# Optimization experiments

Hardware: AMD Instinct MI355X
Metric: run time of the kernel (lower is better)

## Reference

```python
import jax, jax.numpy as jnp
import numpy as np

B, T, H, IN, D = 256, 64, 256, 2, 8

def _gru_cell(x, h, Wih, Whh, bih, bhh):
    gi = x @ Wih.T + bih          # [B,3H]
    gh = h @ Whh.T + bhh
    ir, iz, inn = jnp.split(gi, 3, axis=-1)
    hr, hz, hn = jnp.split(gh, 3, axis=-1)
    r = jax.nn.sigmoid(ir + hr)
    z = jax.nn.sigmoid(iz + hz)
    n = jnp.tanh(inn + r * hn)
    return (1.0 - z) * n + z * h

def _gru2(x, h, p):
    # h: [2,B,H]; p: 8-tuple of layer-0 then layer-1 GRU params
    h0 = _gru_cell(x, h[0], p[0], p[1], p[2], p[3])
    h1 = _gru_cell(h0, h[1], p[4], p[5], p[6], p[7])
    return jnp.stack([h0, h1], axis=0)

def _attend(h_new, buf, i, attn_W, v_W, fc_W, fc_b):
    # h_new: [2,B,H] fresh RNN hidden; buf: [B,T,2,H] history of hiddens
    s = h_new.transpose(1, 0, 2)                            # [B,2,H]
    es = jnp.einsum('blh,gh->blg', s, attn_W[:, :H])        # s half of cat(s,hiddens)
    eh = jnp.einsum('bjlh,gh->bjlg', buf, attn_W[:, H:])    # hiddens half
    energy = jnp.tanh(es[:, None] + eh)                     # [B,T,2,H]
    logits = jnp.einsum('bjlg,og->bjlo', energy, v_W)       # [B,T,2,2]
    mask = (jnp.arange(buf.shape[1]) <= i)[None, :, None, None]
    logits = jnp.where(mask, logits, jnp.float32(-1e30))
    m = logits.max(axis=(1, 2), keepdims=True)              # softmax over all 2*(i+1) history slots
    e = jnp.exp(logits - m)
    a = e / e.sum(axis=(1, 2), keepdims=True)
    c = jnp.einsum('bjlo,bjlh->obh', a, buf)                # [2,B,H] == bmm(a,hiddens).transpose(0,1)
    h_cat = jnp.concatenate([c, h_new], axis=-1)            # [2,B,2H]
    return h_cat @ fc_W.T + fc_b                            # [2,B,H]

def setup_inputs():
    key = jax.random.key(0)
    ks = jax.random.split(key, 32)
    def u(k, shape, fan):
        b = 1.0 / np.sqrt(fan)
        return jax.random.uniform(k, shape, jnp.float32, -b, b)
    inp = {'received': jax.random.normal(ks[0], (B, T, IN), jnp.float32)}
    i = 1
    for g in ('g1', 'g2'):
        inp[g + '_Wih0'] = u(ks[i], (3 * H, IN), H); i += 1
        inp[g + '_Whh0'] = u(ks[i], (3 * H, H), H); i += 1
        inp[g + '_bih0'] = u(ks[i], (3 * H,), H); i += 1
        inp[g + '_bhh0'] = u(ks[i], (3 * H,), H); i += 1
        inp[g + '_Wih1'] = u(ks[i], (3 * H, H), H); i += 1
        inp[g + '_Whh1'] = u(ks[i], (3 * H, H), H); i += 1
        inp[g + '_bih1'] = u(ks[i], (3 * H,), H); i += 1
        inp[g + '_bhh1'] = u(ks[i], (3 * H,), H); i += 1
    inp['fc_W'] = u(ks[i], (H, 2 * H), 2 * H); i += 1
    inp['fc_b'] = u(ks[i], (H,), 2 * H); i += 1
    inp['attn_W'] = u(ks[i], (H, 2 * H), 2 * H); i += 1
    inp['v_W'] = u(ks[i], (2, H), H); i += 1
    inp['out_W'] = u(ks[i], (1, 2 * H), 2 * H); i += 1
    inp['out_b'] = u(ks[i], (1,), 2 * H); i += 1
    return inp

def reference(received, g1_Wih0, g1_Whh0, g1_bih0, g1_bhh0, g1_Wih1, g1_Whh1, g1_bih1, g1_bhh1,
              g2_Wih0, g2_Whh0, g2_bih0, g2_bhh0, g2_Wih1, g2_Whh1, g2_bih1, g2_bhh1,
              fc_W, fc_b, attn_W, v_W, out_W, out_b):
    p1 = (g1_Wih0, g1_Whh0, g1_bih0, g1_bhh0, g1_Wih1, g1_Whh1, g1_bih1, g1_bhh1)
    p2 = (g2_Wih0, g2_Whh0, g2_bih0, g2_bhh0, g2_Wih1, g2_Whh1, g2_bih1, g2_bhh1)
    b, t = received.shape[0], received.shape[1]
    h_init = jnp.zeros((2, b, H), received.dtype)
    buf_init = jnp.zeros((b, t, 2, H), received.dtype)

    def step(carry, inp):
        h1, h2, b1, b2 = carry
        x, i = inp
        h1n = _gru2(x, h1, p1)
        h2n = _gru2(x, h2, p2)
        b1 = b1.at[:, i].set(h1n.transpose(1, 0, 2))
        b2 = b2.at[:, i].set(h2n.transpose(1, 0, 2))
        h1a = _attend(h1n, b1, i, attn_W, v_W, fc_W, fc_b)
        h2a = _attend(h2n, b2, i, attn_W, v_W, fc_W, fc_b)
        return (h1a, h2a, b1, b2), (h1n[1], h2n[1])

    xs = (received.transpose(1, 0, 2), jnp.arange(t))
    _, (o1, o2) = jax.lax.scan(step, (h_init, h_init, buf_init, buf_init), xs)
    out1 = o1.transpose(1, 0, 2)   # [B,T,H] = concat of per-step top-layer GRU outputs
    out2 = o2.transpose(1, 0, 2)
    ar = jnp.arange(t)
    idx = jnp.where(ar >= t - D - 1, t - 1, ar + D)   # delayed stream-2 features
    rnn_out = jnp.concatenate([out1, out2[:, idx]], axis=-1)  # [B,T,2H]
    return jax.nn.sigmoid(rnn_out @ out_W.T + out_b)          # [B,T,1]
```

## Files before the change

kernel.cpp:

```cpp
#include <hip/hip_runtime.h>

#define BATCH 256
#define TT    64
#define HH    256
#define DD    8

#define BW    4
#define NTHR  512
#define NBLK  (2 * (BATCH / BW))

typedef __attribute__((ext_vector_type(8))) short bfrag;
typedef __attribute__((ext_vector_type(4))) float f4;
typedef __attribute__((ext_vector_type(4))) unsigned int uv4;
typedef __attribute__((ext_vector_type(2))) unsigned int uv2;

#define SWZ(g) ((((g) & 31) << 3) | ((g) >> 5))

__device__ __forceinline__ float rcpf(float x) { return __builtin_amdgcn_rcpf(x); }
__device__ __forceinline__ float sigf(float x) { return rcpf(1.0f + __expf(-x)); }
__device__ __forceinline__ float tanh_fast(float x) {
  const float e = __expf(-2.0f * x);
  return __builtin_fmaf(2.0f, rcpf(1.0f + e), -1.0f);
}
__device__ __forceinline__ unsigned short f2bf(float f) {
  union { float f; unsigned int u; } v; v.f = f;
  return (unsigned short)((v.u + 0x7fffu + ((v.u >> 16) & 1u)) >> 16);
}
__device__ __forceinline__ float bf_lo(unsigned int u) {
  union { unsigned int u; float f; } v; v.u = u << 16; return v.f;
}
__device__ __forceinline__ float bf_hi(unsigned int u) {
  union { unsigned int u; float f; } v; v.u = u & 0xffff0000u; return v.f;
}
__device__ __forceinline__ bfrag zero_frag() {
  bfrag r;
#pragma unroll
  for (int x = 0; x < 8; x++) r[x] = 0;
  return r;
}
__device__ __forceinline__ f4 mfma16(bfrag a, bfrag b, f4 c) {
  return __builtin_amdgcn_mfma_f32_16x16x32_bf16(a, b, c, 0, 0, 0);
}

#define W1_ELEMS  196608
#define STACK_W   (3 * W1_ELEMS)
#define B3_OFF    (2 * STACK_W)
#define B4_OFF    (B3_OFF + 131072)
#define WF_TOTAL  (B4_OFF + 131072)

__global__ __launch_bounds__(256) void prep_weights(
    const float* __restrict__ g1_Whh0, const float* __restrict__ g1_Wih1, const float* __restrict__ g1_Whh1,
    const float* __restrict__ g2_Whh0, const float* __restrict__ g2_Wih1, const float* __restrict__ g2_Whh1,
    const float* __restrict__ attn_W, const float* __restrict__ fc_W,
    unsigned short* __restrict__ wf) {
  const int id = blockIdx.x * 256 + threadIdx.x;
  if (id >= WF_TOTAL) return;
  float src;
  if (id < 2 * STACK_W) {
    const int s = id / STACK_W, r = id % STACK_W;
    const int mm = r / W1_ELEMS, e = r % W1_ELEMS;
    const int j = e & 7, lane = (e >> 3) & 63, c = (e >> 9) & 7, t = e >> 12;
    const int nt = t / 3, g = t % 3;
    const int n = nt * 16 + (lane & 15);
    const int k = c * 32 + ((lane >> 4) << 3) + j;
    const float* W = (mm == 0) ? (s ? g2_Whh0 : g1_Whh0)
                   : (mm == 1) ? (s ? g2_Wih1 : g1_Wih1)
                               : (s ? g2_Whh1 : g1_Whh1);
    src = W[(g * 256 + n) * 256 + k];
  } else if (id < B4_OFF) {
    const int e = id - B3_OFF;
    const int j = e & 7, lane = (e >> 3) & 63, c = (e >> 9) & 7, t = e >> 12;
    const int n = t * 16 + (lane & 15);
    const int k = c * 32 + ((lane >> 4) << 3) + j;
    src = (n < 256) ? attn_W[n * 512 + k] : attn_W[(n - 256) * 512 + 256 + k];
  } else {
    const int e = id - B4_OFF;
    const int j = e & 7, lane = (e >> 3) & 63, c = (e >> 9) & 15, t = e >> 13;
    const int n = t * 16 + (lane & 15);
    const int k = c * 32 + ((lane >> 4) << 3) + j;
    src = fc_W[n * 512 + k];
  }
  wf[id] = f2bf(src);
}

__global__ __launch_bounds__(NTHR, 2) void gru_attn(
    const float* __restrict__ received,
    const float* __restrict__ g1_Wih0, const float* __restrict__ g1_bih0, const float* __restrict__ g1_bhh0,
    const float* __restrict__ g1_bih1, const float* __restrict__ g1_bhh1,
    const float* __restrict__ g2_Wih0, const float* __restrict__ g2_bih0, const float* __restrict__ g2_bhh0,
    const float* __restrict__ g2_bih1, const float* __restrict__ g2_bhh1,
    const float* __restrict__ fc_b, const float* __restrict__ v_W, const float* __restrict__ out_W,
    const unsigned short* __restrict__ wf,
    unsigned short* __restrict__ buf_g, unsigned short* __restrict__ ehb_g,
    float* __restrict__ ws_p) {
  const int tid  = threadIdx.x;
  const int lane = tid & 63, wave = tid >> 6;
  const int col  = lane & 15, q = lane >> 4;
  const int s    = blockIdx.x & 1;
  const int b0   = (blockIdx.x >> 1) * BW;

  const float* Wih0 = s ? g2_Wih0 : g1_Wih0;
  const float* bih0 = s ? g2_bih0 : g1_bih0;
  const float* bhh0 = s ? g2_bhh0 : g1_bhh0;
  const float* bih1 = s ? g2_bih1 : g1_bih1;
  const float* bhh1 = s ? g2_bhh1 : g1_bhh1;

  const bfrag* W1  = (const bfrag*)(wf + (size_t)s * STACK_W);
  const bfrag* W2I = W1 + W1_ELEMS / 8;
  const bfrag* W2H = W2I + W1_ELEMS / 8;
  const bfrag* B3  = (const bfrag*)(wf + B3_OFF);
  const bfrag* B4  = (const bfrag*)(wf + B4_OFF);

  unsigned short* buf = buf_g + (size_t)s * BATCH * TT * 2 * HH;
  unsigned short* ehb = ehb_g + (size_t)s * BATCH * TT * 2 * HH;
  float* pp = ws_p + (size_t)s * BATCH * TT;

  float wxr0v[2], wxr1v[2], wxz0v[2], wxz1v[2], wxn0v[2], wxn1v[2];
  float br0v[2], bz0v[2], bni0v[2], bnh0v[2];
  float br1v[2], bz1v[2], bni1v[2], bnh1v[2];
  float fcbv[2], owvv[2];
#pragma unroll
  for (int r2 = 0; r2 < 2; r2++) {
    const int nm = (wave + 8 * r2) * 16 + col;
    wxr0v[r2] = Wih0[nm * 2];         wxr1v[r2] = Wih0[nm * 2 + 1];
    wxz0v[r2] = Wih0[(256 + nm) * 2]; wxz1v[r2] = Wih0[(256 + nm) * 2 + 1];
    wxn0v[r2] = Wih0[(512 + nm) * 2]; wxn1v[r2] = Wih0[(512 + nm) * 2 + 1];
    br0v[r2]  = bih0[nm] + bhh0[nm];
    bz0v[r2]  = bih0[256 + nm] + bhh0[256 + nm];
    bni0v[r2] = bih0[512 + nm]; bnh0v[r2] = bhh0[512 + nm];
    br1v[r2]  = bih1[nm] + bhh1[nm];
    bz1v[r2]  = bih1[256 + nm] + bhh1[256 + nm];
    bni1v[r2] = bih1[512 + nm]; bnh1v[r2] = bhh1[512 + nm];
    fcbv[r2]  = fc_b[nm];
    owvv[r2]  = out_W[s * HH + nm];
  }

  __shared__ float          hf[8 * 260] __attribute__((aligned(16)));
  __shared__ unsigned short hb[8 * 264] __attribute__((aligned(16)));
  __shared__ unsigned short hnb[8 * 264] __attribute__((aligned(16)));
  __shared__ float          es_s[8 * 264] __attribute__((aligned(16)));
  __shared__ unsigned short cacb[8 * 264] __attribute__((aligned(16)));
  __shared__ float          lp[TT * 4 * 2 * 2];
  __shared__ float          vw_s[512];
  __shared__ float          cpart[2 * 2 * 4 * 256] __attribute__((aligned(16)));
  __shared__ float          pw_s[32];
  __shared__ float          sinv_s[8];

  for (int x = tid; x < 8 * 260; x += NTHR) hf[x] = 0.0f;
  for (int x = tid; x < 8 * 264; x += NTHR) hb[x] = 0;
  { const int o = tid >> 8, g = tid & 255; vw_s[o * 256 + SWZ(g)] = v_W[tid]; }
  __syncthreads();

#pragma unroll 1
  for (int i = 0; i < TT; ++i) {
    float2 xv[BW];
#pragma unroll
    for (int b = 0; b < BW; b++) xv[b] = ((const float2*)received)[(size_t)(b0 + b) * TT + i];

    {
      bfrag a0[8];
#pragma unroll
      for (int c = 0; c < 8; c++)
        a0[c] = (col < BW) ? *(const bfrag*)&hb[col * 264 + c * 32 + q * 8] : zero_frag();
#pragma unroll
      for (int r2 = 0; r2 < 2; r2++) {
        const int nt16 = wave + 8 * r2;
        bfrag bb[24];
#pragma unroll
        for (int c = 0; c < 8; c++) {
          bb[c]      = W1[((nt16 * 3 + 0) * 8 + c) * 64 + lane];
          bb[8 + c]  = W1[((nt16 * 3 + 1) * 8 + c) * 64 + lane];
          bb[16 + c] = W1[((nt16 * 3 + 2) * 8 + c) * 64 + lane];
        }
        f4 aR = {0, 0, 0, 0}, aZ = {0, 0, 0, 0}, aN = {0, 0, 0, 0};
#pragma unroll
        for (int c = 0; c < 8; c++) {
          aR = mfma16(a0[c], bb[c], aR);
          aZ = mfma16(a0[c], bb[8 + c], aZ);
          aN = mfma16(a0[c], bb[16 + c], aN);
        }
        if (lane < 16) {
          const int nm = nt16 * 16 + col;
#pragma unroll
          for (int reg = 0; reg < 4; reg++) {
            const int b = reg;
            const float rr = sigf(xv[b].x * wxr0v[r2] + xv[b].y * wxr1v[r2] + br0v[r2] + aR[reg]);
            const float zz = sigf(xv[b].x * wxz0v[r2] + xv[b].y * wxz1v[r2] + bz0v[r2] + aZ[reg]);
            const float nn = tanh_fast(xv[b].x * wxn0v[r2] + xv[b].y * wxn1v[r2] + bni0v[r2] +
                                       rr * (aN[reg] + bnh0v[r2]));
            const float hn0 = (1.0f - zz) * nn + zz * hf[b * 260 + nm];
            const unsigned short hv = f2bf(hn0);
            hnb[b * 264 + nm] = hv;
            buf[((size_t)(b0 + b) * (TT * 2) + i * 2 + 0) * HH + nm] = hv;
          }
        }
      }
    }
    __syncthreads();

    {
      bfrag ai[8], ah[8];
#pragma unroll
      for (int c = 0; c < 8; c++) {
        ai[c] = (col < BW) ? *(const bfrag*)&hnb[col * 264 + c * 32 + q * 8] : zero_frag();
        ah[c] = (col < BW) ? *(const bfrag*)&hb[(4 + col) * 264 + c * 32 + q * 8] : zero_frag();
      }
      float pv[4] = {0.f, 0.f, 0.f, 0.f};
#pragma unroll
      for (int r2 = 0; r2 < 2; r2++) {
        const int nt16 = wave + 8 * r2;
        bfrag bb[24];
#pragma unroll
        for (int c = 0; c < 8; c++) {
          bb[c]      = W2I[((nt16 * 3 + 0) * 8 + c) * 64 + lane];
          bb[8 + c]  = W2I[((nt16 * 3 + 1) * 8 + c) * 64 + lane];
          bb[16 + c] = W2I[((nt16 * 3 + 2) * 8 + c) * 64 + lane];
        }
        f4 iR = {0, 0, 0, 0}, iZ = {0, 0, 0, 0}, iN = {0, 0, 0, 0};
#pragma unroll
        for (int c = 0; c < 8; c++) {
          iR = mfma16(ai[c], bb[c], iR);
          iZ = mfma16(ai[c], bb[8 + c], iZ);
          iN = mfma16(ai[c], bb[16 + c], iN);
        }
#pragma unroll
        for (int c = 0; c < 8; c++) {
          bb[c]      = W2H[((nt16 * 3 + 0) * 8 + c) * 64 + lane];
          bb[8 + c]  = W2H[((nt16 * 3 + 1) * 8 + c) * 64 + lane];
          bb[16 + c] = W2H[((nt16 * 3 + 2) * 8 + c) * 64 + lane];
        }
        f4 hR = {0, 0, 0, 0}, hZ = {0, 0, 0, 0}, hN = {0, 0, 0, 0};
#pragma unroll
        for (int c = 0; c < 8; c++) {
          hR = mfma16(ah[c], bb[c], hR);
          hZ = mfma16(ah[c], bb[8 + c], hZ);
          hN = mfma16(ah[c], bb[16 + c], hN);
        }
        if (lane < 16) {
          const int nm = nt16 * 16 + col;
#pragma unroll
          for (int reg = 0; reg < 4; reg++) {
            const int b = reg;
            const float rr = sigf(iR[reg] + hR[reg] + br1v[r2]);
            const float zz = sigf(iZ[reg] + hZ[reg] + bz1v[r2]);
            const float nn = tanh_fast(iN[reg] + bni1v[r2] + rr * (hN[reg] + bnh1v[r2]));
            const float hn1 = (1.0f - zz) * nn + zz * hf[(4 + b) * 260 + nm];
            const unsigned short hv = f2bf(hn1);
            hnb[(4 + b) * 264 + nm] = hv;
            buf[((size_t)(b0 + b) * (TT * 2) + i * 2 + 1) * HH + nm] = hv;
            pv[reg] += hn1 * owvv[r2];
          }
        }
      }
#pragma unroll
      for (int reg = 0; reg < 4; reg++) {
#pragma unroll
        for (int d = 1; d < 16; d <<= 1) pv[reg] += __shfl_xor(pv[reg], d, 64);
      }
      if (lane == 0) {
#pragma unroll
        for (int reg = 0; reg < 4; reg++) pw_s[wave * 4 + reg] = pv[reg];
      }
    }
    __syncthreads();

    {
      bfrag a3[8];
#pragma unroll
      for (int c = 0; c < 8; c++)
        a3[c] = (col < 8) ? *(const bfrag*)&hnb[col * 264 + c * 32 + q * 8] : zero_frag();
#pragma unroll
      for (int tt = 0; tt < 4; tt++) {
        const int t = wave * 4 + tt;
        bfrag bb[8];
#pragma unroll
        for (int c = 0; c < 8; c++) bb[c] = B3[(t * 8 + c) * 64 + lane];
        f4 acc = {0, 0, 0, 0};
#pragma unroll
        for (int c = 0; c < 8; c++) acc = mfma16(a3[c], bb[c], acc);
        if (lane < 32) {
          const int n = t * 16 + col;
#pragma unroll
          for (int reg = 0; reg < 4; reg++) {
            const int m = q * 4 + reg;
            const int l = m >> 2, b = m & 3;
            if (t < 16) es_s[(b * 2 + l) * 264 + SWZ(n)] = acc[reg];
            else ehb[((size_t)(b0 + b) * (TT * 2) + i * 2 + l) * HH + (n - 256)] = f2bf(acc[reg]);
          }
        }
      }
      if (tid < 4) {
        float ss = 0.0f;
#pragma unroll
        for (int w = 0; w < 8; w++) ss += pw_s[w * 4 + tid];
        pp[(size_t)(b0 + tid) * TT + i] = ss;
      }
    }
    __syncthreads();

    {
      const int nslot = 64 * (i + 1);
      int slot = tid;
      uv4 cur[4];
      if (slot < nslot) {
        const uv4* ep = (const uv4*)(ehb + ((size_t)(b0 + ((slot >> 3) & 3)) * (TT * 2) +
                                            (slot >> 6) * 2 + ((slot >> 5) & 1)) * HH + (slot & 7) * 32);
#pragma unroll
        for (int u = 0; u < 4; u++) cur[u] = __builtin_nontemporal_load(ep + u);
      }
      for (; slot < nslot; slot += NTHR) {
        const int snext = slot + NTHR;
        uv4 nxt[4];
        if (snext < nslot) {
          const uv4* ep2 = (const uv4*)(ehb + ((size_t)(b0 + ((snext >> 3) & 3)) * (TT * 2) +
                                               (snext >> 6) * 2 + ((snext >> 5) & 1)) * HH + (snext & 7) * 32);
#pragma unroll
          for (int u = 0; u < 4; u++) nxt[u] = __builtin_nontemporal_load(ep2 + u);
        } else {
#pragma unroll
          for (int u = 0; u < 4; u++) nxt[u] = cur[u];
        }
        const int g8 = slot & 7;
        const int b  = (slot >> 3) & 3;
        const int l  = (slot >> 5) & 1;
        const int j  = slot >> 6;
        const int eb = (b * 2 + l) * 264;
        float l0 = 0.0f, l1 = 0.0f;
#pragma unroll
        for (int u = 0; u < 4; u++) {
#pragma unroll
          for (int k = 0; k < 4; k++) {
            const int m = u * 8 + k * 2;
            const float e0 = tanh_fast(es_s[eb + (m * 8 + g8)] + bf_lo(cur[u][k]));
            const float e1 = tanh_fast(es_s[eb + ((m + 1) * 8 + g8)] + bf_hi(cur[u][k]));
            l0 = fmaf(e0, vw_s[m * 8 + g8], fmaf(e1, vw_s[(m + 1) * 8 + g8], l0));
            l1 = fmaf(e0, vw_s[256 + m * 8 + g8], fmaf(e1, vw_s[256 + (m + 1) * 8 + g8], l1));
          }
        }
#pragma unroll
        for (int d = 1; d < 8; d <<= 1) { l0 += __shfl_xor(l0, d, 64); l1 += __shfl_xor(l1, d, 64); }
        if (g8 == 0) {
          lp[((j * 4 + b) * 2 + l) * 2 + 0] = __expf(l0);
          lp[((j * 4 + b) * 2 + l) * 2 + 1] = __expf(l1);
        }
#pragma unroll
        for (int u = 0; u < 4; u++) cur[u] = nxt[u];
      }
    }
    __syncthreads();

    {
      {
        const int b = wave >> 1, o = wave & 1;
        const int jl2 = 2 * (i + 1);
        const int jl0 = lane, jl1 = lane + 64;
        float sa = 0.0f;
        if (jl0 < jl2) sa += lp[((jl0 >> 1) * 4 + b) * 4 + (jl0 & 1) * 2 + o];
        if (jl1 < jl2) sa += lp[((jl1 >> 1) * 4 + b) * 4 + (jl1 & 1) * 2 + o];
#pragma unroll
        for (int d = 1; d < 64; d <<= 1) sa += __shfl_xor(sa, d, 64);
        if (lane == 0) sinv_s[b * 2 + o] = rcpf(sa);
      }
      const int h4   = tid & 63;
      const int jpar = (tid >> 6) & 1;
      const int cb   = tid >> 7;
      const uv2* bp = (const uv2*)(buf + ((size_t)(b0 + cb) * (TT * 2)) * HH);
      float c00 = 0.f, c01 = 0.f, c02 = 0.f, c03 = 0.f;
      float c10 = 0.f, c11 = 0.f, c12 = 0.f, c13 = 0.f;
      uv2 aj0 = {0, 0}, aj1 = {0, 0}, bj0 = {0, 0}, bj1 = {0, 0};
      int j = jpar;
      if (j <= i) {
        aj0 = __builtin_nontemporal_load(bp + (j * 2 + 0) * 64 + h4);
        aj1 = __builtin_nontemporal_load(bp + (j * 2 + 1) * 64 + h4);
        bj0 = __builtin_nontemporal_load(bp + ((j + 2) * 2 + 0) * 64 + h4);
        bj1 = __builtin_nontemporal_load(bp + ((j + 2) * 2 + 1) * 64 + h4);
      }
      for (; j <= i; j += 2) {
        uv2 cj0 = {0, 0}, cj1 = {0, 0};
        if (j + 4 <= i) {
          cj0 = __builtin_nontemporal_load(bp + ((j + 4) * 2 + 0) * 64 + h4);
          cj1 = __builtin_nontemporal_load(bp + ((j + 4) * 2 + 1) * 64 + h4);
        }
#pragma unroll
        for (int l = 0; l < 2; l++) {
          const uv2 u = l ? aj1 : aj0;
          const float e0 = lp[((j * 4 + cb) * 2 + l) * 2 + 0];
          const float e1 = lp[((j * 4 + cb) * 2 + l) * 2 + 1];
          const float v0 = bf_lo(u[0]), v1 = bf_hi(u[0]);
          const float v2 = bf_lo(u[1]), v3 = bf_hi(u[1]);
          c00 = fmaf(e0, v0, c00); c01 = fmaf(e0, v1, c01);
          c02 = fmaf(e0, v2, c02); c03 = fmaf(e0, v3, c03);
          c10 = fmaf(e1, v0, c10); c11 = fmaf(e1, v1, c11);
          c12 = fmaf(e1, v2, c12); c13 = fmaf(e1, v3, c13);
        }
        aj0 = bj0; aj1 = bj1; bj0 = cj0; bj1 = cj1;
      }
      ((float4*)&cpart[((jpar * 2 + 0) * 4 + cb) * 256])[h4] = make_float4(c00, c01, c02, c03);
      ((float4*)&cpart[((jpar * 2 + 1) * 4 + cb) * 256])[h4] = make_float4(c10, c11, c12, c13);
    }
    __syncthreads();

    for (int x = tid; x < 2 * BW * HH; x += NTHR) {
      const int g = x & 255, b = (x >> 8) & 3, o = x >> 10;
      const float v = (cpart[(o * 4 + b) * 256 + g] + cpart[((2 + o) * 4 + b) * 256 + g]) *
                      sinv_s[b * 2 + o];
      cacb[(o * 4 + b) * 264 + g] = f2bf(v);
    }
    __syncthreads();

    {
      bfrag a4[16];
      if (col < 8) {
#pragma unroll
        for (int c = 0; c < 8; c++) {
          a4[c]     = *(const bfrag*)&cacb[col * 264 + c * 32 + q * 8];
          a4[c + 8] = *(const bfrag*)&hnb[col * 264 + c * 32 + q * 8];
        }
      } else {
#pragma unroll
        for (int c = 0; c < 16; c++) a4[c] = zero_frag();
      }
#pragma unroll
      for (int r2 = 0; r2 < 2; r2++) {
        const int t16 = wave + 8 * r2;
        bfrag bb[16];
#pragma unroll
        for (int c = 0; c < 16; c++) bb[c] = B4[(t16 * 16 + c) * 64 + lane];
        f4 acc = {0, 0, 0, 0};
#pragma unroll
        for (int c = 0; c < 16; c++) acc = mfma16(a4[c], bb[c], acc);
        if (lane < 32) {
          const int nm = t16 * 16 + col;
#pragma unroll
          for (int reg = 0; reg < 4; reg++) {
            const int m = q * 4 + reg;
            const float v = acc[reg] + fcbv[r2];
            hf[m * 260 + nm] = v;
            hb[m * 264 + nm] = f2bf(v);
          }
        }
      }
    }
    __syncthreads();
  }
}

__global__ __launch_bounds__(256) void final_combine(const float* __restrict__ ws_p,
                                                     const float* __restrict__ out_b,
                                                     float* __restrict__ out) {
  const int gidx = blockIdx.x * blockDim.x + threadIdx.x;
  if (gidx >= BATCH * TT) return;
  const int b = gidx >> 6;
  const int t = gidx & 63;
  const int idx = (t >= TT - DD - 1) ? (TT - 1) : (t + DD);
  const float* p1 = ws_p;
  const float* p2 = ws_p + (size_t)BATCH * TT;
  const float v = p1[(size_t)b * TT + t] + p2[(size_t)b * TT + idx] + out_b[0];
  out[gidx] = 1.0f / (1.0f + __expf(-v));
}

extern "C" void kernel_launch(void* const* d_in, const int* in_sizes, int n_in,
                              void* d_out, int out_size, void* d_ws, size_t ws_size,
                              hipStream_t stream) {
  const float* received = (const float*)d_in[0];
  const float* g1_Wih0 = (const float*)d_in[1];
  const float* g1_Whh0 = (const float*)d_in[2];
  const float* g1_bih0 = (const float*)d_in[3];
  const float* g1_bhh0 = (const float*)d_in[4];
  const float* g1_Wih1 = (const float*)d_in[5];
  const float* g1_Whh1 = (const float*)d_in[6];
  const float* g1_bih1 = (const float*)d_in[7];
  const float* g1_bhh1 = (const float*)d_in[8];
  const float* g2_Wih0 = (const float*)d_in[9];
  const float* g2_Whh0 = (const float*)d_in[10];
  const float* g2_bih0 = (const float*)d_in[11];
  const float* g2_bhh0 = (const float*)d_in[12];
  const float* g2_Wih1 = (const float*)d_in[13];
  const float* g2_Whh1 = (const float*)d_in[14];
  const float* g2_bih1 = (const float*)d_in[15];
  const float* g2_bhh1 = (const float*)d_in[16];
  const float* fc_W   = (const float*)d_in[17];
  const float* fc_b   = (const float*)d_in[18];
  const float* attn_W = (const float*)d_in[19];
  const float* v_W    = (const float*)d_in[20];
  const float* out_W  = (const float*)d_in[21];
  const float* out_b  = (const float*)d_in[22];

  float* ws_p = (float*)d_ws;
  unsigned short* buf = (unsigned short*)(ws_p + 2 * BATCH * TT);
  unsigned short* ehb = buf + (size_t)2 * BATCH * TT * 2 * HH;
  unsigned short* wf  = ehb + (size_t)2 * BATCH * TT * 2 * HH;

  hipLaunchKernelGGL(prep_weights, dim3((WF_TOTAL + 255) / 256), dim3(256), 0, stream,
                     g1_Whh0, g1_Wih1, g1_Whh1, g2_Whh0, g2_Wih1, g2_Whh1,
                     attn_W, fc_W, wf);

  hipLaunchKernelGGL(gru_attn, dim3(NBLK), dim3(NTHR), 0, stream,
                     received,
                     g1_Wih0, g1_bih0, g1_bhh0, g1_bih1, g1_bhh1,
                     g2_Wih0, g2_bih0, g2_bhh0, g2_bih1, g2_bhh1,
                     fc_b, v_W, out_W, wf, buf, ehb, ws_p);

  hipLaunchKernelGGL(final_combine, dim3((BATCH * TT + 255) / 256), dim3(256), 0, stream,
                     ws_p, out_b, (float*)d_out);
}
```

Before: 5.926 ms.

## Halve batch per block and keep hidden history buffer in LDS

Drops the batch rows per block from 4 to 2, which doubles the grid to 256 blocks, and keeps each block's full hidden-state history (64×2×2×256 bf16, 128 KB) in shared memory instead of global memory. The context-vector accumulation now reads that LDS history directly, with one thread per (batch, h) pair, and folds the softmax normalisation sum into the same loop. This removes the cpart/sinv staging and one barrier. The ehb stores become nontemporal. The cost is that half the MFMA rows sit unused in each 16-row tile, the weights are streamed again per block twice as often, and the large LDS footprint probably limits occupancy to one block per CU.

New measurement: 8.111 ms. 36.9% more time.

```diff
diff --git a/kernel.cpp b/kernel.cpp
--- a/kernel.cpp
+++ b/kernel.cpp
@@ -5,14 +5,13 @@
 #define HH    256
 #define DD    8
 
-#define BW    4
+#define BW    2
 #define NTHR  512
 #define NBLK  (2 * (BATCH / BW))
 
 typedef __attribute__((ext_vector_type(8))) short bfrag;
 typedef __attribute__((ext_vector_type(4))) float f4;
 typedef __attribute__((ext_vector_type(4))) unsigned int uv4;
-typedef __attribute__((ext_vector_type(2))) unsigned int uv2;
 
 #define SWZ(g) ((((g) & 31) << 3) | ((g) >> 5))
 
@@ -25,6 +24,9 @@
 __device__ __forceinline__ unsigned short f2bf(float f) {
   union { float f; unsigned int u; } v; v.f = f;
   return (unsigned short)((v.u + 0x7fffu + ((v.u >> 16) & 1u)) >> 16);
+}
+__device__ __forceinline__ float bf2f(unsigned short u) {
+  union { unsigned int u; float f; } v; v.u = ((unsigned int)u) << 16; return v.f;
 }
 __device__ __forceinline__ float bf_lo(unsigned int u) {
   union { unsigned int u; float f; } v; v.u = u << 16; return v.f;
@@ -91,8 +93,7 @@
     const float* __restrict__ g2_bih1, const float* __restrict__ g2_bhh1,
     const float* __restrict__ fc_b, const float* __restrict__ v_W, const float* __restrict__ out_W,
     const unsigned short* __restrict__ wf,
-    unsigned short* __restrict__ buf_g, unsigned short* __restrict__ ehb_g,
-    float* __restrict__ ws_p) {
+    unsigned short* __restrict__ ehb_g, float* __restrict__ ws_p) {
   const int tid  = threadIdx.x;
   const int lane = tid & 63, wave = tid >> 6;
   const int col  = lane & 15, q = lane >> 4;
@@ -111,7 +112,6 @@
   const bfrag* B3  = (const bfrag*)(wf + B3_OFF);
   const bfrag* B4  = (const bfrag*)(wf + B4_OFF);
 
-  unsigned short* buf = buf_g + (size_t)s * BATCH * TT * 2 * HH;
   unsigned short* ehb = ehb_g + (size_t)s * BATCH * TT * 2 * HH;
   float* pp = ws_p + (size_t)s * BATCH * TT;
 
@@ -135,19 +135,18 @@
     owvv[r2]  = out_W[s * HH + nm];
   }
 
-  __shared__ float          hf[8 * 260] __attribute__((aligned(16)));
-  __shared__ unsigned short hb[8 * 264] __attribute__((aligned(16)));
-  __shared__ unsigned short hnb[8 * 264] __attribute__((aligned(16)));
-  __shared__ float          es_s[8 * 264] __attribute__((aligned(16)));
-  __shared__ unsigned short cacb[8 * 264] __attribute__((aligned(16)));
-  __shared__ float          lp[TT * 4 * 2 * 2];
+  __shared__ unsigned short bufL[TT * 2 * 2 * 256];
+  __shared__ float          hf[4 * 260] __attribute__((aligned(16)));
+  __shared__ unsigned short hb[4 * 264] __attribute__((aligned(16)));
+  __shared__ unsigned short hnb[4 * 264] __attribute__((aligned(16)));
+  __shared__ float          es_s[4 * 264] __attribute__((aligned(16)));
+  __shared__ unsigned short cacb[4 * 264] __attribute__((aligned(16)));
+  __shared__ float          lp[TT * 2 * 2 * 2];
   __shared__ float          vw_s[512];
-  __shared__ float          cpart[2 * 2 * 4 * 256] __attribute__((aligned(16)));
-  __shared__ float          pw_s[32];
-  __shared__ float          sinv_s[8];
-
-  for (int x = tid; x < 8 * 260; x += NTHR) hf[x] = 0.0f;
-  for (int x = tid; x < 8 * 264; x += NTHR) hb[x] = 0;
+  __shared__ float          pw_s[16];
+
+  for (int x = tid; x < 4 * 260; x += NTHR) hf[x] = 0.0f;
+  for (int x = tid; x < 4 * 264; x += NTHR) hb[x] = 0;
   { const int o = tid >> 8, g = tid & 255; vw_s[o * 256 + SWZ(g)] = v_W[tid]; }
   __syncthreads();
 
@@ -182,7 +181,7 @@
         if (lane < 16) {
           const int nm = nt16 * 16 + col;
 #pragma unroll
-          for (int reg = 0; reg < 4; reg++) {
+          for (int reg = 0; reg < BW; reg++) {
             const int b = reg;
             const float rr = sigf(xv[b].x * wxr0v[r2] + xv[b].y * wxr1v[r2] + br0v[r2] + aR[reg]);
             const float zz = sigf(xv[b].x * wxz0v[r2] + xv[b].y * wxz1v[r2] + bz0v[r2] + aZ[reg]);
@@ -191,7 +190,7 @@
             const float hn0 = (1.0f - zz) * nn + zz * hf[b * 260 + nm];
             const unsigned short hv = f2bf(hn0);
             hnb[b * 264 + nm] = hv;
-            buf[((size_t)(b0 + b) * (TT * 2) + i * 2 + 0) * HH + nm] = hv;
+            bufL[((i * 2 + 0) * 2 + b) * 256 + nm] = hv;
           }
         }
       }
@@ -203,9 +202,9 @@
 #pragma unroll
       for (int c = 0; c < 8; c++) {
         ai[c] = (col < BW) ? *(const bfrag*)&hnb[col * 264 + c * 32 + q * 8] : zero_frag();
-        ah[c] = (col < BW) ? *(const bfrag*)&hb[(4 + col) * 264 + c * 32 + q * 8] : zero_frag();
-      }
-      float pv[4] = {0.f, 0.f, 0.f, 0.f};
+        ah[c] = (col < BW) ? *(const bfrag*)&hb[(2 + col) * 264 + c * 32 + q * 8] : zero_frag();
+      }
+      float pv[BW] = {0.f, 0.f};
 #pragma unroll
       for (int r2 = 0; r2 < 2; r2++) {
         const int nt16 = wave + 8 * r2;
@@ -239,27 +238,27 @@
         if (lane < 16) {
           const int nm = nt16 * 16 + col;
 #pragma unroll
-          for (int reg = 0; reg < 4; reg++) {
+          for (int reg = 0; reg < BW; reg++) {
             const int b = reg;
             const float rr = sigf(iR[reg] + hR[reg] + br1v[r2]);
             const float zz = sigf(iZ[reg] + hZ[reg] + bz1v[r2]);
             const float nn = tanh_fast(iN[reg] + bni1v[r2] + rr * (hN[reg] + bnh1v[r2]));
-            const float hn1 = (1.0f - zz) * nn + zz * hf[(4 + b) * 260 + nm];
+            const float hn1 = (1.0f - zz) * nn + zz * hf[(2 + b) * 260 + nm];
             const unsigned short hv = f2bf(hn1);
-            hnb[(4 + b) * 264 + nm] = hv;
-            buf[((size_t)(b0 + b) * (TT * 2) + i * 2 + 1) * HH + nm] = hv;
+            hnb[(2 + b) * 264 + nm] = hv;
+            bufL[((i * 2 + 1) * 2 + b) * 256 + nm] = hv;
             pv[reg] += hn1 * owvv[r2];
           }
         }
       }
 #pragma unroll
-      for (int reg = 0; reg < 4; reg++) {
+      for (int reg = 0; reg < BW; reg++) {
 #pragma unroll
         for (int d = 1; d < 16; d <<= 1) pv[reg] += __shfl_xor(pv[reg], d, 64);
       }
       if (lane == 0) {
 #pragma unroll
-        for (int reg = 0; reg < 4; reg++) pw_s[wave * 4 + reg] = pv[reg];
+        for (int reg = 0; reg < BW; reg++) pw_s[wave * 2 + reg] = pv[reg];
       }
     }
     __syncthreads();
@@ -268,7 +267,7 @@
       bfrag a3[8];
 #pragma unroll
       for (int c = 0; c < 8; c++)
-        a3[c] = (col < 8) ? *(const bfrag*)&hnb[col * 264 + c * 32 + q * 8] : zero_frag();
+        a3[c] = (col < 4) ? *(const bfrag*)&hnb[col * 264 + c * 32 + q * 8] : zero_frag();
 #pragma unroll
       for (int tt = 0; tt < 4; tt++) {
         const int t = wave * 4 + tt;
@@ -278,33 +277,34 @@
         f4 acc = {0, 0, 0, 0};
 #pragma unroll
         for (int c = 0; c < 8; c++) acc = mfma16(a3[c], bb[c], acc);
-        if (lane < 32) {
+        if (lane < 16) {
           const int n = t * 16 + col;
 #pragma unroll
           for (int reg = 0; reg < 4; reg++) {
-            const int m = q * 4 + reg;
-            const int l = m >> 2, b = m & 3;
+            const int l = reg >> 1, b = reg & 1;
             if (t < 16) es_s[(b * 2 + l) * 264 + SWZ(n)] = acc[reg];
-            else ehb[((size_t)(b0 + b) * (TT * 2) + i * 2 + l) * HH + (n - 256)] = f2bf(acc[reg]);
+            else __builtin_nontemporal_store(
+                     f2bf(acc[reg]),
+                     &ehb[((size_t)(b0 + b) * (TT * 2) + i * 2 + l) * HH + (n - 256)]);
           }
         }
       }
-      if (tid < 4) {
+      if (tid < BW) {
         float ss = 0.0f;
 #pragma unroll
-        for (int w = 0; w < 8; w++) ss += pw_s[w * 4 + tid];
+        for (int w = 0; w < 8; w++) ss += pw_s[w * 2 + tid];
         pp[(size_t)(b0 + tid) * TT + i] = ss;
       }
     }
     __syncthreads();
 
     {
-      const int nslot = 64 * (i + 1);
+      const int nslot = 32 * (i + 1);
       int slot = tid;
       uv4 cur[4];
       if (slot < nslot) {
-        const uv4* ep = (const uv4*)(ehb + ((size_t)(b0 + ((slot >> 3) & 3)) * (TT * 2) +
-                                            (slot >> 6) * 2 + ((slot >> 5) & 1)) * HH + (slot & 7) * 32);
+        const uv4* ep = (const uv4*)(ehb + ((size_t)(b0 + ((slot >> 3) & 1)) * (TT * 2) +
+                                            (slot >> 5) * 2 + ((slot >> 4) & 1)) * HH + (slot & 7) * 32);
 #pragma unroll
         for (int u = 0; u < 4; u++) cur[u] = __builtin_nontemporal_load(ep + u);
       }
@@ -312,8 +312,8 @@
         const int snext = slot + NTHR;
         uv4 nxt[4];
         if (snext < nslot) {
-          const uv4* ep2 = (const uv4*)(ehb + ((size_t)(b0 + ((snext >> 3) & 3)) * (TT * 2) +
-                                               (snext >> 6) * 2 + ((snext >> 5) & 1)) * HH + (snext & 7) * 32);
+          const uv4* ep2 = (const uv4*)(ehb + ((size_t)(b0 + ((snext >> 3) & 1)) * (TT * 2) +
+                                               (snext >> 5) * 2 + ((snext >> 4) & 1)) * HH + (snext & 7) * 32);
 #pragma unroll
           for (int u = 0; u < 4; u++) nxt[u] = __builtin_nontemporal_load(ep2 + u);
         } else {
@@ -321,9 +321,9 @@
           for (int u = 0; u < 4; u++) nxt[u] = cur[u];
         }
         const int g8 = slot & 7;
-        const int b  = (slot >> 3) & 3;
-        const int l  = (slot >> 5) & 1;
-        const int j  = slot >> 6;
+        const int b  = (slot >> 3) & 1;
+        const int l  = (slot >> 4) & 1;
+        const int j  = slot >> 5;
         const int eb = (b * 2 + l) * 264;
         float l0 = 0.0f, l1 = 0.0f;
 #pragma unroll
@@ -340,8 +340,8 @@
 #pragma unroll
         for (int d = 1; d < 8; d <<= 1) { l0 += __shfl_xor(l0, d, 64); l1 += __shfl_xor(l1, d, 64); }
         if (g8 == 0) {
-          lp[((j * 4 + b) * 2 + l) * 2 + 0] = __expf(l0);
-          lp[((j * 4 + b) * 2 + l) * 2 + 1] = __expf(l1);
+          lp[((j * 2 + b) * 2 + l) * 2 + 0] = __expf(l0);
+          lp[((j * 2 + b) * 2 + l) * 2 + 1] = __expf(l1);
         }
 #pragma unroll
         for (int u = 0; u < 4; u++) cur[u] = nxt[u];
@@ -350,67 +350,27 @@
     __syncthreads();
 
     {
-      {
-        const int b = wave >> 1, o = wave & 1;
-        const int jl2 = 2 * (i + 1);
-        const int jl0 = lane, jl1 = lane + 64;
-        float sa = 0.0f;
-        if (jl0 < jl2) sa += lp[((jl0 >> 1) * 4 + b) * 4 + (jl0 & 1) * 2 + o];
-        if (jl1 < jl2) sa += lp[((jl1 >> 1) * 4 + b) * 4 + (jl1 & 1) * 2 + o];
-#pragma unroll
-        for (int d = 1; d < 64; d <<= 1) sa += __shfl_xor(sa, d, 64);
-        if (lane == 0) sinv_s[b * 2 + o] = rcpf(sa);
-      }
-      const int h4   = tid & 63;
-      const int jpar = (tid >> 6) & 1;
-      const int cb   = tid >> 7;
-      const uv2* bp = (const uv2*)(buf + ((size_t)(b0 + cb) * (TT * 2)) * HH);
-      float c00 = 0.f, c01 = 0.f, c02 = 0.f, c03 = 0.f;
-      float c10 = 0.f, c11 = 0.f, c12 = 0.f, c13 = 0.f;
-      uv2 aj0 = {0, 0}, aj1 = {0, 0}, bj0 = {0, 0}, bj1 = {0, 0};
-      int j = jpar;
-      if (j <= i) {
-        aj0 = __builtin_nontemporal_load(bp + (j * 2 + 0) * 64 + h4);
-        aj1 = __builtin_nontemporal_load(bp + (j * 2 + 1) * 64 + h4);
-        bj0 = __builtin_nontemporal_load(bp + ((j + 2) * 2 + 0) * 64 + h4);
-        bj1 = __builtin_nontemporal_load(bp + ((j + 2) * 2 + 1) * 64 + h4);
-      }
-      for (; j <= i; j += 2) {
-        uv2 cj0 = {0, 0}, cj1 = {0, 0};
-        if (j + 4 <= i) {
-          cj0 = __builtin_nontemporal_load(bp + ((j + 4) * 2 + 0) * 64 + h4);
-          cj1 = __builtin_nontemporal_load(bp + ((j + 4) * 2 + 1) * 64 + h4);
-        }
+      const int cb = tid >> 8;
+      const int h  = tid & 255;
+      float c0 = 0.f, c1 = 0.f, ss0 = 0.f, ss1 = 0.f;
+      for (int j = 0; j <= i; j++) {
 #pragma unroll
         for (int l = 0; l < 2; l++) {
-          const uv2 u = l ? aj1 : aj0;
-          const float e0 = lp[((j * 4 + cb) * 2 + l) * 2 + 0];
-          const float e1 = lp[((j * 4 + cb) * 2 + l) * 2 + 1];
-          const float v0 = bf_lo(u[0]), v1 = bf_hi(u[0]);
-          const float v2 = bf_lo(u[1]), v3 = bf_hi(u[1]);
-          c00 = fmaf(e0, v0, c00); c01 = fmaf(e0, v1, c01);
-          c02 = fmaf(e0, v2, c02); c03 = fmaf(e0, v3, c03);
-          c10 = fmaf(e1, v0, c10); c11 = fmaf(e1, v1, c11);
-          c12 = fmaf(e1, v2, c12); c13 = fmaf(e1, v3, c13);
-        }
-        aj0 = bj0; aj1 = bj1; bj0 = cj0; bj1 = cj1;
-      }
-      ((float4*)&cpart[((jpar * 2 + 0) * 4 + cb) * 256])[h4] = make_float4(c00, c01, c02, c03);
-      ((float4*)&cpart[((jpar * 2 + 1) * 4 + cb) * 256])[h4] = make_float4(c10, c11, c12, c13);
-    }
-    __syncthreads();
-
-    for (int x = tid; x < 2 * BW * HH; x += NTHR) {
-      const int g = x & 255, b = (x >> 8) & 3, o = x >> 10;
-      const float v = (cpart[(o * 4 + b) * 256 + g] + cpart[((2 + o) * 4 + b) * 256 + g]) *
-                      sinv_s[b * 2 + o];
-      cacb[(o * 4 + b) * 264 + g] = f2bf(v);
+          const float v  = bf2f(bufL[((j * 2 + l) * 2 + cb) * 256 + h]);
+          const float e0 = lp[((j * 2 + cb) * 2 + l) * 2 + 0];
+          const float e1 = lp[((j * 2 + cb) * 2 + l) * 2 + 1];
+          c0 = fmaf(e0, v, c0); c1 = fmaf(e1, v, c1);
+          ss0 += e0; ss1 += e1;
+        }
+      }
+      cacb[(0 * 2 + cb) * 264 + h] = f2bf(c0 * rcpf(ss0));
+      cacb[(1 * 2 + cb) * 264 + h] = f2bf(c1 * rcpf(ss1));
     }
     __syncthreads();
 
     {
       bfrag a4[16];
-      if (col < 8) {
+      if (col < 4) {
 #pragma unroll
         for (int c = 0; c < 8; c++) {
           a4[c]     = *(const bfrag*)&cacb[col * 264 + c * 32 + q * 8];
@@ -429,14 +389,13 @@
         f4 acc = {0, 0, 0, 0};
 #pragma unroll
         for (int c = 0; c < 16; c++) acc = mfma16(a4[c], bb[c], acc);
-        if (lane < 32) {
+        if (lane < 16) {
           const int nm = t16 * 16 + col;
 #pragma unroll
           for (int reg = 0; reg < 4; reg++) {
-            const int m = q * 4 + reg;
             const float v = acc[reg] + fcbv[r2];
-            hf[m * 260 + nm] = v;
-            hb[m * 264 + nm] = f2bf(v);
+            hf[reg * 260 + nm] = v;
+            hb[reg * 264 + nm] = f2bf(v);
           }
         }
       }
@@ -487,8 +446,7 @@
   const float* out_b  = (const float*)d_in[22];
 
   float* ws_p = (float*)d_ws;
-  unsigned short* buf = (unsigned short*)(ws_p + 2 * BATCH * TT);
-  unsigned short* ehb = buf + (size_t)2 * BATCH * TT * 2 * HH;
+  unsigned short* ehb = (unsigned short*)(ws_p + 2 * BATCH * TT);
   unsigned short* wf  = ehb + (size_t)2 * BATCH * TT * 2 * HH;
 
   hipLaunchKernelGGL(prep_weights, dim3((WF_TOTAL + 255) / 256), dim3(256), 0, stream,
@@ -499,7 +457,7 @@
                      received,
                      g1_Wih0, g1_bih0, g1_bhh0, g1_bih1, g1_bhh1,
                      g2_Wih0, g2_bih0, g2_bhh0, g2_bih1, g2_bhh1,
-                     fc_b, v_W, out_W, wf, buf, ehb, ws_p);
+                     fc_b, v_W, out_W, wf, ehb, ws_p);
 
   hipLaunchKernelGGL(final_combine, dim3((BATCH * TT + 255) / 256), dim3(256), 0, stream,
                      ws_p, out_b, (float*)d_out);
```
